# Kernel tuning notes

Hardware: AMD Instinct MI355X
Metric: run time of the kernel (lower is better)

## Reference

```python
import jax, jax.numpy as jnp
import numpy as np

DIM = 128
HIDDEN = 384  # int(32 * ((128*3 + 31) // 32))
B = 4
N_DATA = 100000
E = 200000
N_LOGICAL = 4096
EPS = 1e-05


def _rmsnorm(x, w):
    return x * jax.lax.rsqrt(jnp.mean(x * x, axis=-1, keepdims=True) + EPS) * w


def _ffn(x, w1, w2, w3):
    return (jax.nn.silu(x @ w1) * (x @ w3)) @ w2


def setup_inputs() -> dict:
    key = jax.random.key(0)
    ks = jax.random.split(key, 12)
    s = 0.02
    inp = {
        "v": jax.random.normal(ks[0], (B, N_DATA, DIM), dtype=jnp.float32),
        "data_src": jax.random.randint(ks[1], (E,), 0, N_DATA, dtype=jnp.int32),
        "data_dst": jax.random.randint(ks[2], (E,), 0, N_LOGICAL, dtype=jnp.int32),
        "num_logical": N_LOGICAL,
        # data_update params (RMSNorm + SwiGLU FFN)
        "rms1_w": jnp.ones((DIM,), jnp.float32),
        "w1a": jax.random.normal(ks[3], (DIM, HIDDEN), jnp.float32) * s,
        "w2a": jax.random.normal(ks[4], (HIDDEN, DIM), jnp.float32) * s,
        "w3a": jax.random.normal(ks[5], (DIM, HIDDEN), jnp.float32) * s,
        # logical_update params
        "rms2_w": jnp.ones((DIM,), jnp.float32),
        "w1b": jax.random.normal(ks[6], (DIM, HIDDEN), jnp.float32) * s,
        "w2b": jax.random.normal(ks[7], (HIDDEN, DIM), jnp.float32) * s,
        "w3b": jax.random.normal(ks[8], (DIM, HIDDEN), jnp.float32) * s,
        # out_proj (Linear(dim, 1))
        "wout": jax.random.normal(ks[9], (DIM, 1), jnp.float32) * s,
        "bout": jnp.zeros((1,), jnp.float32),
    }
    return inp


def reference(v, data_src, data_dst, num_logical, rms1_w, w1a, w2a, w3a,
              rms2_w, w1b, w2b, w3b, wout, bout):
    # v_act = tanh(data_update(v) + v)
    v_act = jnp.tanh(_ffn(_rmsnorm(v, rms1_w), w1a, w2a, w3a) + v)
    # gather data nodes, scatter-multiply into logical nodes (identity = 1)
    gathered = v_act[:, data_src, :]  # [B, E, D]
    l = jax.vmap(lambda g: jax.ops.segment_prod(g, data_dst, num_segments=num_logical))(gathered)  # [B, NL, D]
    l = _ffn(_rmsnorm(l, rms2_w), w1b, w2b, w3b) + l
    return (l @ wout + bout)[..., 0]  # [B, NL]
```

## Files before the change

### kernel.cpp

```cpp
#include <hip/hip_runtime.h>
#include <hip/hip_bf16.h>

#define DIM 128
#define HIDDEN 384
#define BATCH 4
#define NDATA 100000
#define NEDGE 200000
#define NLOG 4096

typedef __bf16 bf16x8 __attribute__((ext_vector_type(8)));
typedef __bf16 bf16x2 __attribute__((ext_vector_type(2)));
typedef float f32x4 __attribute__((ext_vector_type(4)));
typedef unsigned short u16;
typedef unsigned int u32;

__device__ __forceinline__ u16 f2bf(float f) {
  __bf16 b = (__bf16)f;
  return __builtin_bit_cast(u16, b);
}
__device__ __forceinline__ u32 pk2bf(float lo, float hi) {
  bf16x2 t;
  t[0] = (__bf16)lo;
  t[1] = (__bf16)hi;
  return __builtin_bit_cast(u32, t);
}
__device__ __forceinline__ bf16x8 as_bf(uint4 u) {
  return __builtin_bit_cast(bf16x8, u);
}
__device__ __forceinline__ float fast_tanh(float x) {
  float xc = fminf(fmaxf(x, -15.f), 15.f);
  float t = __expf(2.f * xc);
  return (t - 1.f) * __builtin_amdgcn_rcpf(t + 1.f);
}

__global__ void zero_counts_kernel(int* __restrict__ counts) {
  int i = blockIdx.x * blockDim.x + threadIdx.x;
  if (i < NLOG) counts[i] = 0;
}

__global__ void count_kernel(const int* __restrict__ dst, int* __restrict__ counts) {
  int e = blockIdx.x * blockDim.x + threadIdx.x;
  if (e < NEDGE) atomicAdd(&counts[dst[e]], 1);
}

__global__ __launch_bounds__(1024) void scan_kernel(const int* __restrict__ counts,
                                                    int* __restrict__ offsets,
                                                    int* __restrict__ cursor) {
  __shared__ int sdata[1024];
  const int t = threadIdx.x;
  const int c0 = counts[4 * t + 0];
  const int c1 = counts[4 * t + 1];
  const int c2 = counts[4 * t + 2];
  const int c3 = counts[4 * t + 3];
  const int s = c0 + c1 + c2 + c3;
  sdata[t] = s;
  __syncthreads();
  for (int off = 1; off < 1024; off <<= 1) {
    int vv = (t >= off) ? sdata[t - off] : 0;
    __syncthreads();
    sdata[t] += vv;
    __syncthreads();
  }
  const int excl = sdata[t] - s;
  const int o0 = excl, o1 = o0 + c0, o2 = o1 + c1, o3 = o2 + c2;
  offsets[4 * t + 0] = o0;
  offsets[4 * t + 1] = o1;
  offsets[4 * t + 2] = o2;
  offsets[4 * t + 3] = o3;
  cursor[4 * t + 0] = o0;
  cursor[4 * t + 1] = o1;
  cursor[4 * t + 2] = o2;
  cursor[4 * t + 3] = o3;
  if (t == 1023) offsets[NLOG] = o3 + c3;
}

__global__ void scatter_kernel(const int* __restrict__ src, const int* __restrict__ dst,
                               int* __restrict__ cursor, int* __restrict__ sorted_src) {
  int e = blockIdx.x * blockDim.x + threadIdx.x;
  if (e < NEDGE) {
    int d = dst[e];
    int pos = atomicAdd(&cursor[d], 1);
    sorted_src[pos] = src[e];
  }
}

__device__ __forceinline__ void prod_accum(uint4 u, f32x4& plo, f32x4& phi) {
  f32x4 lo, hi;
  lo[0] = __uint_as_float(u.x << 16);
  lo[1] = __uint_as_float(u.x & 0xffff0000u);
  lo[2] = __uint_as_float(u.y << 16);
  lo[3] = __uint_as_float(u.y & 0xffff0000u);
  hi[0] = __uint_as_float(u.z << 16);
  hi[1] = __uint_as_float(u.z & 0xffff0000u);
  hi[2] = __uint_as_float(u.w << 16);
  hi[3] = __uint_as_float(u.w & 0xffff0000u);
  plo *= lo;
  phi *= hi;
}

__global__ __launch_bounds__(64) void prod_kernel_t(const u16* __restrict__ va,
                                                    const int* __restrict__ offsets,
                                                    const int* __restrict__ sorted_src,
                                                    float* __restrict__ l) {
  const int s = blockIdx.x;
  const int c = threadIdx.x;
  const int beg = offsets[s];
  const int end = offsets[s + 1];
  const u16* base = va + 8 * c;
  f32x4 plo[8], phi[8];
#pragma unroll
  for (int i = 0; i < 8; ++i) {
    plo[i] = {1.f, 1.f, 1.f, 1.f};
    phi[i] = {1.f, 1.f, 1.f, 1.f};
  }
  int e = beg;
  for (; e < end && (e & 3); ++e) {
    const uint4 u = *(const uint4*)(base + (size_t)sorted_src[e] * 512);
    prod_accum(u, plo[0], phi[0]);
  }
  for (; e + 8 <= end; e += 8) {
    const int4 ia = *(const int4*)(sorted_src + e);
    const int4 ib = *(const int4*)(sorted_src + e + 4);
    const int idx[8] = {ia.x, ia.y, ia.z, ia.w, ib.x, ib.y, ib.z, ib.w};
    uint4 r[8];
#pragma unroll
    for (int i = 0; i < 8; ++i) r[i] = *(const uint4*)(base + (size_t)idx[i] * 512);
#pragma unroll
    for (int i = 0; i < 8; ++i) prod_accum(r[i], plo[i], phi[i]);
  }
  for (; e < end; ++e) {
    const uint4 u = *(const uint4*)(base + (size_t)sorted_src[e] * 512);
    prod_accum(u, plo[0], phi[0]);
  }
  const f32x4 rlo =
      ((plo[0] * plo[1]) * (plo[2] * plo[3])) * ((plo[4] * plo[5]) * (plo[6] * plo[7]));
  const f32x4 rhi =
      ((phi[0] * phi[1]) * (phi[2] * phi[3])) * ((phi[4] * phi[5]) * (phi[6] * phi[7]));
  float* outp = l + ((size_t)(c >> 4) * NLOG + s) * DIM + (c & 15) * 8;
  *(f32x4*)outp = rlo;
  *(f32x4*)(outp + 4) = rhi;
}

__global__ __launch_bounds__(256) void convert_w_kernel(
    const float* __restrict__ w1a, const float* __restrict__ w3a,
    const float* __restrict__ w2a, const float* __restrict__ w1b,
    const float* __restrict__ w3b, const float* __restrict__ w2b,
    u16* __restrict__ w1Ta, u16* __restrict__ w3Ta, u16* __restrict__ w2Ta,
    u16* __restrict__ w1Tb, u16* __restrict__ w3Tb, u16* __restrict__ w2Tb) {
  const int i = blockIdx.x * 256 + threadIdx.x;
  const int n1 = i >> 7, k1 = i & 127;
  w1Ta[i] = f2bf(w1a[k1 * HIDDEN + n1]);
  w3Ta[i] = f2bf(w3a[k1 * HIDDEN + n1]);
  w1Tb[i] = f2bf(w1b[k1 * HIDDEN + n1]);
  w3Tb[i] = f2bf(w3b[k1 * HIDDEN + n1]);
  const int n2 = i / HIDDEN, k2 = i - n2 * HIDDEN;
  w2Ta[i] = f2bf(w2a[k2 * DIM + n2]);
  w2Tb[i] = f2bf(w2b[k2 * DIM + n2]);
}

__global__ __launch_bounds__(256, 3) void ffn_mfma_kernel(
    const float* __restrict__ xin, const float* __restrict__ rmsw,
    const u16* __restrict__ w1T, const u16* __restrict__ w3T,
    const u16* __restrict__ w2T, float* __restrict__ xout, int mode) {
  __shared__ alignas(16) u16 sm[24576];
  char* const sb = (char*)sm;
  const int t = threadIdx.x;
  const int row0 = blockIdx.x * 64;

  {
    const int r = t >> 2;
    const int q = t & 3;
    const float* vr = xin + (size_t)(row0 + r) * DIM + q * 32;
    float av[32];
#pragma unroll
    for (int i = 0; i < 8; ++i) *(float4*)(av + 4 * i) = *(const float4*)(vr + 4 * i);
    float wr_[32];
#pragma unroll
    for (int i = 0; i < 8; ++i)
      *(float4*)(wr_ + 4 * i) = *(const float4*)(rmsw + q * 32 + 4 * i);
    float ss = 0.f;
#pragma unroll
    for (int i = 0; i < 32; ++i) ss += av[i] * av[i];
    ss += __shfl_xor(ss, 1);
    ss += __shfl_xor(ss, 2);
    const float scale = __builtin_amdgcn_rsqf(ss * (1.0f / DIM) + 1e-5f);
    const int r7 = r & 7;
#pragma unroll
    for (int i = 0; i < 4; ++i) {
      uint4 pk;
      pk.x = pk2bf(av[8 * i + 0] * scale * wr_[8 * i + 0],
                   av[8 * i + 1] * scale * wr_[8 * i + 1]);
      pk.y = pk2bf(av[8 * i + 2] * scale * wr_[8 * i + 2],
                   av[8 * i + 3] * scale * wr_[8 * i + 3]);
      pk.z = pk2bf(av[8 * i + 4] * scale * wr_[8 * i + 4],
                   av[8 * i + 5] * scale * wr_[8 * i + 5]);
      pk.w = pk2bf(av[8 * i + 6] * scale * wr_[8 * i + 6],
                   av[8 * i + 7] * scale * wr_[8 * i + 7]);
      const int c = q * 4 + i;
      *(uint4*)(sb + r * 256 + ((c ^ r7) << 4)) = pk;
    }
  }
  __syncthreads();

  const int wv = t >> 6;
  const int lane = t & 63;
  const int m16 = lane & 15;
  const int quad = lane >> 4;
  const int m7 = m16 & 7;

  uint4 bfr[4][4];
#pragma unroll
  for (int nt = 0; nt < 4; ++nt) {
    const int row = nt * 16 + m16;
#pragma unroll
    for (int ks = 0; ks < 4; ++ks)
      bfr[nt][ks] = *(const uint4*)(sb + row * 256 + (((4 * ks + quad) ^ m7) << 4));
  }
  __syncthreads();

  const int woff = wv * 96;
#pragma unroll 1
  for (int mt = 0; mt < 6; ++mt) {
    const size_t wrow = (size_t)(woff + mt * 16 + m16) * DIM + quad * 8;
    uint4 a1[4], a3[4];
#pragma unroll
    for (int ks = 0; ks < 4; ++ks) {
      a1[ks] = *(const uint4*)(w1T + wrow + ks * 32);
      a3[ks] = *(const uint4*)(w3T + wrow + ks * 32);
    }
    f32x4 acc1[4] = {{0.f, 0.f, 0.f, 0.f}, {0.f, 0.f, 0.f, 0.f},
                     {0.f, 0.f, 0.f, 0.f}, {0.f, 0.f, 0.f, 0.f}};
    f32x4 acc3[4] = {{0.f, 0.f, 0.f, 0.f}, {0.f, 0.f, 0.f, 0.f},
                     {0.f, 0.f, 0.f, 0.f}, {0.f, 0.f, 0.f, 0.f}};
#pragma unroll
    for (int ks = 0; ks < 4; ++ks) {
      const bf16x8 fa1 = as_bf(a1[ks]);
      const bf16x8 fa3 = as_bf(a3[ks]);
#pragma unroll
      for (int nt = 0; nt < 4; ++nt) {
        const bf16x8 fb = as_bf(bfr[nt][ks]);
        acc1[nt] = __builtin_amdgcn_mfma_f32_16x16x32_bf16(fa1, fb, acc1[nt], 0, 0, 0);
        acc3[nt] = __builtin_amdgcn_mfma_f32_16x16x32_bf16(fa3, fb, acc3[nt], 0, 0, 0);
      }
    }
    const int hch = (woff + mt * 16) >> 3;
    const int chu = (hch + (quad >> 1));
    const int half = (quad & 1) * 8;
#pragma unroll
    for (int nt = 0; nt < 4; ++nt) {
      const int row = nt * 16 + m16;
      float g[4];
#pragma unroll
      for (int r = 0; r < 4; ++r) {
        const float h1 = acc1[nt][r], h3 = acc3[nt][r];
        g[r] = h1 * __builtin_amdgcn_rcpf(1.0f + __expf(-h1)) * h3;
      }
      uint2 pk;
      pk.x = pk2bf(g[0], g[1]);
      pk.y = pk2bf(g[2], g[3]);
      *(uint2*)(sb + row * 768 + ((chu ^ m7) << 4) + half) = pk;
    }
  }
  __syncthreads();

#pragma unroll 1
  for (int mt = 0; mt < 2; ++mt) {
    const size_t wrow = (size_t)(wv * 32 + mt * 16 + m16) * HIDDEN + quad * 8;
    uint4 aw[12];
#pragma unroll
    for (int ks = 0; ks < 12; ++ks) aw[ks] = *(const uint4*)(w2T + wrow + ks * 32);
#pragma unroll 1
    for (int nt = 0; nt < 4; ++nt) {
      const int row = nt * 16 + m16;
      uint4 bg[12];
#pragma unroll
      for (int ks = 0; ks < 12; ++ks)
        bg[ks] = *(const uint4*)(sb + row * 768 + (((4 * ks + quad) ^ m7) << 4));
      f32x4 acc = {0.f, 0.f, 0.f, 0.f};
#pragma unroll
      for (int ks = 0; ks < 12; ++ks)
        acc = __builtin_amdgcn_mfma_f32_16x16x32_bf16(as_bf(aw[ks]), as_bf(bg[ks]), acc,
                                                      0, 0, 0);
      const int grow = row0 + row;
      const int d0 = wv * 32 + mt * 16 + quad * 4;
      const float4 res = *(const float4*)(xin + (size_t)grow * DIM + d0);
      float4 o;
      o.x = acc[0] + res.x;
      o.y = acc[1] + res.y;
      o.z = acc[2] + res.z;
      o.w = acc[3] + res.w;
      if (mode) {
        o.x = fast_tanh(o.x);
        o.y = fast_tanh(o.y);
        o.z = fast_tanh(o.z);
        o.w = fast_tanh(o.w);
        const int b = grow / NDATA;
        const int i = grow - b * NDATA;
        u16* const xb = (u16*)xout;
        uint2 pk;
        pk.x = pk2bf(o.x, o.y);
        pk.y = pk2bf(o.z, o.w);
        *(uint2*)(xb + ((size_t)i * BATCH + b) * DIM + d0) = pk;
      } else {
        *(float4*)(xout + (size_t)grow * DIM + d0) = o;
      }
    }
  }
}

__global__ __launch_bounds__(256) void readout_kernel(const float* __restrict__ fbuf,
                                                      const float* __restrict__ wout,
                                                      const float* __restrict__ bout,
                                                      float* __restrict__ out) {
  const int t = threadIdx.x;
  const int row = blockIdx.x * 4 + (t >> 6);
  const int lane = t & 63;
  const float2 f = *(const float2*)(fbuf + (size_t)row * DIM + lane * 2);
  const float2 w = *(const float2*)(wout + lane * 2);
  float s = f.x * w.x + f.y * w.y;
  s += __shfl_xor(s, 1);
  s += __shfl_xor(s, 2);
  s += __shfl_xor(s, 4);
  s += __shfl_xor(s, 8);
  s += __shfl_xor(s, 16);
  s += __shfl_xor(s, 32);
  if (lane == 0) out[row] = s + bout[0];
}

extern "C" void kernel_launch(void* const* d_in, const int* in_sizes, int n_in,
                              void* d_out, int out_size, void* d_ws, size_t ws_size,
                              hipStream_t stream) {
  const float* v = (const float*)d_in[0];
  const int* data_src = (const int*)d_in[1];
  const int* data_dst = (const int*)d_in[2];
  const float* rms1_w = (const float*)d_in[4];
  const float* w1a = (const float*)d_in[5];
  const float* w2a = (const float*)d_in[6];
  const float* w3a = (const float*)d_in[7];
  const float* rms2_w = (const float*)d_in[8];
  const float* w1b = (const float*)d_in[9];
  const float* w2b = (const float*)d_in[10];
  const float* w3b = (const float*)d_in[11];
  const float* wout = (const float*)d_in[12];
  const float* bout = (const float*)d_in[13];
  float* out = (float*)d_out;

  char* ws = (char*)d_ws;
  size_t off = 0;
  auto take = [&](size_t bytes) -> char* {
    char* p = ws + off;
    off += (bytes + 255) & ~(size_t)255;
    return p;
  };
  u16* v_act_t = (u16*)take((size_t)BATCH * NDATA * DIM * 2);
  float* lbuf = (float*)take((size_t)BATCH * NLOG * DIM * 4);
  float* fbuf = (float*)take((size_t)BATCH * NLOG * DIM * 4);
  int* counts = (int*)take(NLOG * 4);
  int* offsets = (int*)take((NLOG + 1) * 4);
  int* cursor = (int*)take(NLOG * 4);
  int* sorted_src = (int*)take(NEDGE * 4);
  u16* w1Ta = (u16*)take(HIDDEN * DIM * 2);
  u16* w3Ta = (u16*)take(HIDDEN * DIM * 2);
  u16* w2Ta = (u16*)take(HIDDEN * DIM * 2);
  u16* w1Tb = (u16*)take(HIDDEN * DIM * 2);
  u16* w3Tb = (u16*)take(HIDDEN * DIM * 2);
  u16* w2Tb = (u16*)take(HIDDEN * DIM * 2);

  convert_w_kernel<<<(HIDDEN * DIM) / 256, 256, 0, stream>>>(
      w1a, w3a, w2a, w1b, w3b, w2b, w1Ta, w3Ta, w2Ta, w1Tb, w3Tb, w2Tb);
  zero_counts_kernel<<<(NLOG + 255) / 256, 256, 0, stream>>>(counts);
  count_kernel<<<(NEDGE + 255) / 256, 256, 0, stream>>>(data_dst, counts);
  scan_kernel<<<1, 1024, 0, stream>>>(counts, offsets, cursor);
  scatter_kernel<<<(NEDGE + 255) / 256, 256, 0, stream>>>(data_src, data_dst, cursor,
                                                          sorted_src);
  ffn_mfma_kernel<<<(BATCH * NDATA) / 64, 256, 0, stream>>>(
      v, rms1_w, w1Ta, w3Ta, w2Ta, (float*)v_act_t, 1);
  prod_kernel_t<<<NLOG, 64, 0, stream>>>(v_act_t, offsets, sorted_src, lbuf);
  ffn_mfma_kernel<<<(BATCH * NLOG) / 64, 256, 0, stream>>>(lbuf, rms2_w, w1Tb, w3Tb,
                                                           w2Tb, fbuf, 0);
  readout_kernel<<<(BATCH * NLOG) / 4, 256, 0, stream>>>(fbuf, wout, bout, out);
}
```

Before: 628.7 us.

## Split segment product across four waves and prefetch FFN weight fragments

The segment-product kernel now runs four waves per logical node. Each wave takes a quarter of the edge range, and the partial products are combined through shared memory, which adds memory-level parallelism to the gather. In the FFN kernel the w1/w3 fragments for the next m-tile are loaded while the current tile's MFMAs run, and the residual loads are hoisted out of the inner loop. The trade-off is more registers, an extra barrier, and a different multiplication order in the product.

```diff
diff --git a/kernel.cpp b/kernel.cpp
--- a/kernel.cpp
+++ b/kernel.cpp
@@ -98,14 +98,20 @@
   phi *= hi;
 }
 
-__global__ __launch_bounds__(64) void prod_kernel_t(const u16* __restrict__ va,
-                                                    const int* __restrict__ offsets,
-                                                    const int* __restrict__ sorted_src,
-                                                    float* __restrict__ l) {
+__global__ __launch_bounds__(256) void prod_kernel_t(const u16* __restrict__ va,
+                                                     const int* __restrict__ offsets,
+                                                     const int* __restrict__ sorted_src,
+                                                     float* __restrict__ l) {
+  __shared__ f32x4 part[3][64][2];
   const int s = blockIdx.x;
-  const int c = threadIdx.x;
+  const int t = threadIdx.x;
+  const int w = t >> 6;
+  const int c = t & 63;
   const int beg = offsets[s];
   const int end = offsets[s + 1];
+  const int len = end - beg;
+  const int qb = beg + ((len * w) >> 2);
+  const int qe = beg + ((len * (w + 1)) >> 2);
   const u16* base = va + 8 * c;
   f32x4 plo[8], phi[8];
 #pragma unroll
@@ -113,12 +119,12 @@
     plo[i] = {1.f, 1.f, 1.f, 1.f};
     phi[i] = {1.f, 1.f, 1.f, 1.f};
   }
-  int e = beg;
-  for (; e < end && (e & 3); ++e) {
+  int e = qb;
+  for (; e < qe && (e & 3); ++e) {
     const uint4 u = *(const uint4*)(base + (size_t)sorted_src[e] * 512);
     prod_accum(u, plo[0], phi[0]);
   }
-  for (; e + 8 <= end; e += 8) {
+  for (; e + 8 <= qe; e += 8) {
     const int4 ia = *(const int4*)(sorted_src + e);
     const int4 ib = *(const int4*)(sorted_src + e + 4);
     const int idx[8] = {ia.x, ia.y, ia.z, ia.w, ib.x, ib.y, ib.z, ib.w};
@@ -128,17 +134,29 @@
 #pragma unroll
     for (int i = 0; i < 8; ++i) prod_accum(r[i], plo[i], phi[i]);
   }
-  for (; e < end; ++e) {
+  for (; e < qe; ++e) {
     const uint4 u = *(const uint4*)(base + (size_t)sorted_src[e] * 512);
     prod_accum(u, plo[0], phi[0]);
   }
-  const f32x4 rlo =
+  f32x4 rlo =
       ((plo[0] * plo[1]) * (plo[2] * plo[3])) * ((plo[4] * plo[5]) * (plo[6] * plo[7]));
-  const f32x4 rhi =
+  f32x4 rhi =
       ((phi[0] * phi[1]) * (phi[2] * phi[3])) * ((phi[4] * phi[5]) * (phi[6] * phi[7]));
-  float* outp = l + ((size_t)(c >> 4) * NLOG + s) * DIM + (c & 15) * 8;
-  *(f32x4*)outp = rlo;
-  *(f32x4*)(outp + 4) = rhi;
+  if (w) {
+    part[w - 1][c][0] = rlo;
+    part[w - 1][c][1] = rhi;
+  }
+  __syncthreads();
+  if (w == 0) {
+#pragma unroll
+    for (int i = 0; i < 3; ++i) {
+      rlo *= part[i][c][0];
+      rhi *= part[i][c][1];
+    }
+    float* outp = l + ((size_t)(c >> 4) * NLOG + s) * DIM + (c & 15) * 8;
+    *(f32x4*)outp = rlo;
+    *(f32x4*)(outp + 4) = rhi;
+  }
 }
 
 __global__ __launch_bounds__(256) void convert_w_kernel(
@@ -219,15 +237,17 @@
   __syncthreads();
 
   const int woff = wv * 96;
+  uint4 a1[4], a3[4];
+  {
+    const size_t wrow0 = (size_t)(woff + m16) * DIM + quad * 8;
+#pragma unroll
+    for (int ks = 0; ks < 4; ++ks) {
+      a1[ks] = *(const uint4*)(w1T + wrow0 + ks * 32);
+      a3[ks] = *(const uint4*)(w3T + wrow0 + ks * 32);
+    }
+  }
 #pragma unroll 1
   for (int mt = 0; mt < 6; ++mt) {
-    const size_t wrow = (size_t)(woff + mt * 16 + m16) * DIM + quad * 8;
-    uint4 a1[4], a3[4];
-#pragma unroll
-    for (int ks = 0; ks < 4; ++ks) {
-      a1[ks] = *(const uint4*)(w1T + wrow + ks * 32);
-      a3[ks] = *(const uint4*)(w3T + wrow + ks * 32);
-    }
     f32x4 acc1[4] = {{0.f, 0.f, 0.f, 0.f}, {0.f, 0.f, 0.f, 0.f},
                      {0.f, 0.f, 0.f, 0.f}, {0.f, 0.f, 0.f, 0.f}};
     f32x4 acc3[4] = {{0.f, 0.f, 0.f, 0.f}, {0.f, 0.f, 0.f, 0.f},
@@ -241,6 +261,14 @@
         const bf16x8 fb = as_bf(bfr[nt][ks]);
         acc1[nt] = __builtin_amdgcn_mfma_f32_16x16x32_bf16(fa1, fb, acc1[nt], 0, 0, 0);
         acc3[nt] = __builtin_amdgcn_mfma_f32_16x16x32_bf16(fa3, fb, acc3[nt], 0, 0, 0);
+      }
+    }
+    if (mt < 5) {
+      const size_t wrown = (size_t)(woff + (mt + 1) * 16 + m16) * DIM + quad * 8;
+#pragma unroll
+      for (int ks = 0; ks < 4; ++ks) {
+        a1[ks] = *(const uint4*)(w1T + wrown + ks * 32);
+        a3[ks] = *(const uint4*)(w3T + wrown + ks * 32);
       }
     }
     const int hch = (woff + mt * 16) >> 3;
@@ -266,9 +294,14 @@
 #pragma unroll 1
   for (int mt = 0; mt < 2; ++mt) {
     const size_t wrow = (size_t)(wv * 32 + mt * 16 + m16) * HIDDEN + quad * 8;
+    const int d0 = wv * 32 + mt * 16 + quad * 4;
     uint4 aw[12];
 #pragma unroll
     for (int ks = 0; ks < 12; ++ks) aw[ks] = *(const uint4*)(w2T + wrow + ks * 32);
+    float4 res[4];
+#pragma unroll
+    for (int nt = 0; nt < 4; ++nt)
+      res[nt] = *(const float4*)(xin + (size_t)(row0 + nt * 16 + m16) * DIM + d0);
 #pragma unroll 1
     for (int nt = 0; nt < 4; ++nt) {
       const int row = nt * 16 + m16;
@@ -282,13 +315,11 @@
         acc = __builtin_amdgcn_mfma_f32_16x16x32_bf16(as_bf(aw[ks]), as_bf(bg[ks]), acc,
                                                       0, 0, 0);
       const int grow = row0 + row;
-      const int d0 = wv * 32 + mt * 16 + quad * 4;
-      const float4 res = *(const float4*)(xin + (size_t)grow * DIM + d0);
       float4 o;
-      o.x = acc[0] + res.x;
-      o.y = acc[1] + res.y;
-      o.z = acc[2] + res.z;
-      o.w = acc[3] + res.w;
+      o.x = acc[0] + res[nt].x;
+      o.y = acc[1] + res[nt].y;
+      o.z = acc[2] + res[nt].z;
+      o.w = acc[3] + res[nt].w;
       if (mode) {
         o.x = fast_tanh(o.x);
         o.y = fast_tanh(o.y);
@@ -375,7 +406,7 @@
                                                           sorted_src);
   ffn_mfma_kernel<<<(BATCH * NDATA) / 64, 256, 0, stream>>>(
       v, rms1_w, w1Ta, w3Ta, w2Ta, (float*)v_act_t, 1);
-  prod_kernel_t<<<NLOG, 64, 0, stream>>>(v_act_t, offsets, sorted_src, lbuf);
+  prod_kernel_t<<<NLOG, 256, 0, stream>>>(v_act_t, offsets, sorted_src, lbuf);
   ffn_mfma_kernel<<<(BATCH * NLOG) / 64, 256, 0, stream>>>(lbuf, rms2_w, w1Tb, w3Tb,
                                                            w2Tb, fbuf, 0);
   readout_kernel<<<(BATCH * NLOG) / 4, 256, 0, stream>>>(fbuf, wout, bout, out);
```

Measured after the change: 664.8 us. 1.06x slower.
